# Kernel optimization log

Hardware: AMD Instinct MI355X
Metric: run time of the kernel (lower is better)

Reference implementation:

```python
import jax, jax.numpy as jnp
import numpy as np

N = 100000
E = 3200000

def gcn_conv(x, W, b, src, dst, num_nodes):
    # PyG GCNConv: x' = D^-1/2 (A+I) D^-1/2 (x W) + b
    h = x @ W  # [N, out]
    # self loops appended
    src_sl = jnp.concatenate([src, jnp.arange(num_nodes)])
    dst_sl = jnp.concatenate([dst, jnp.arange(num_nodes)])
    deg = jnp.zeros((num_nodes,), h.dtype).at[dst_sl].add(1.0)
    dinv = jnp.where(deg > 0, 1.0 / jnp.sqrt(deg), 0.0)
    norm = dinv[src_sl] * dinv[dst_sl]  # [E+N]
    msgs = h[src_sl] * norm[:, None]
    out = jnp.zeros_like(h).at[dst_sl].add(msgs)
    return out + b

def setup_inputs() -> dict:
    key = jax.random.key(0)
    k1, k2, k3, k4, k5 = jax.random.split(key, 5)
    z = jax.random.normal(k1, (N, 16), dtype=jnp.float32)
    edge_index = jax.random.randint(k2, (2, E), 0, N, dtype=jnp.int64)
    W1 = jax.random.normal(k3, (16, 256), dtype=jnp.float32) * (1.0 / np.sqrt(16))
    b1 = jnp.zeros((256,), jnp.float32)
    W2 = jax.random.normal(k4, (256, 256), dtype=jnp.float32) * (1.0 / np.sqrt(256))
    b2 = jnp.zeros((256,), jnp.float32)
    return {"z": z, "edge_index": edge_index, "W1": W1, "b1": b1, "W2": W2, "b2": b2}

def reference(z, edge_index, W1, b1, W2, b2):
    src, dst = edge_index[0], edge_index[1]
    h = gcn_conv(z, W1, b1, src, dst, N)
    h = gcn_conv(h, W2, b2, src, dst, N)
    value = jnp.sum(h[src] * h[dst], axis=1)  # [E]
    return jax.nn.sigmoid(value)
```

## Files before the change

kernel.cpp:

```cpp
#include <hip/hip_runtime.h>
#include <hip/hip_fp16.h>
#include <math.h>

#define N_NODES 100000
#define N_EDGES 3200000
#define GRID_N 391
#define GRID_G 6250
#define NSB 782
#define SB_NODES 128
#define SBCAP 5120
#define E_BLK 12800
#define PART_BLOCKS 250
#define PART_THREADS 1024
#define QUART_E 800000
#define GRID_D 3125

#define OFF_DINV 0
#define OFF_C    100016
#define OFF_ZS16 200032
#define OFF_T16  1000048
#define OFF_U    1800064
#define OFF_YT   3400080
#define OFF_ST   4200080
#define OFF_PR   6604720
#define OFF_PB   6604736
#define OFF_ABG  6604752
#define OFF_L    6604768
#define FLOAT_TOTAL 6605024
#define IOFF_GCUR 0
#define IOFF_BEG  1024
#define IOFF_CNT  101024
#define IOFF_BUF  201024
#define IOFF_CSR  4204864

__device__ inline float4 h4_to_f4(uint2 v) {
    __half2 a = *reinterpret_cast<__half2*>(&v.x);
    __half2 b = *reinterpret_cast<__half2*>(&v.y);
    float2 fa = __half22float2(a), fb = __half22float2(b);
    return make_float4(fa.x, fa.y, fb.x, fb.y);
}
__device__ inline uint2 f4_to_h4(float4 f) {
    uint2 r;
    __half2 a = __floats2half2_rn(f.x, f.y);
    __half2 b = __floats2half2_rn(f.z, f.w);
    r.x = *reinterpret_cast<unsigned*>(&a);
    r.y = *reinterpret_cast<unsigned*>(&b);
    return r;
}
__device__ inline float4 pack_h8(float4 a, float4 b) {
    float4 r;
    __half2* p = reinterpret_cast<__half2*>(&r);
    p[0] = __floats2half2_rn(a.x, a.y);
    p[1] = __floats2half2_rn(a.z, a.w);
    p[2] = __floats2half2_rn(b.x, b.y);
    p[3] = __floats2half2_rn(b.z, b.w);
    return r;
}
__device__ inline unsigned h2bits(float a, float b) {
    __half2 h = __floats2half2_rn(a, b);
    return *reinterpret_cast<unsigned*>(&h);
}
__device__ inline float2 bits2f2(unsigned v) {
    __half2 h = *reinterpret_cast<__half2*>(&v);
    return __half22float2(h);
}
__device__ inline float hdot8f(float4 a, float4 b) {
    const __half2* pa = reinterpret_cast<const __half2*>(&a);
    const __half2* pb = reinterpret_cast<const __half2*>(&b);
    float s = 0.0f;
    #pragma unroll
    for (int i = 0; i < 4; i++) {
        float2 fa = __half22float2(pa[i]);
        float2 fb = __half22float2(pb[i]);
        s += fa.x * fb.x + fa.y * fb.y;
    }
    return s;
}

__global__ void __launch_bounds__(PART_THREADS)
k_part(const int* __restrict__ src, const int* __restrict__ dst,
       int* __restrict__ gcur, int* __restrict__ buf) {
    __shared__ int hist[4][NSB];
    __shared__ int cur[NSB];
    int t = threadIdx.x;
    int cp = t >> 8;
    int base = blockIdx.x * E_BLK;
    for (int i = t; i < 4 * NSB; i += PART_THREADS) ((int*)hist)[i] = 0;
    __syncthreads();
    for (int i = t; i < E_BLK; i += PART_THREADS) {
        int e = base + i;
        if (e < N_EDGES)
            atomicAdd(&hist[cp][__builtin_nontemporal_load(dst + e) >> 7], 1);
    }
    __syncthreads();
    for (int i = t; i < NSB; i += PART_THREADS) {
        int h = hist[0][i] + hist[1][i] + hist[2][i] + hist[3][i];
        cur[i] = (h > 0) ? atomicAdd(&gcur[i], h) : 0;
    }
    __syncthreads();
    for (int i = t; i < E_BLK; i += PART_THREADS) {
        int e = base + i;
        if (e >= N_EDGES) continue;
        int d = __builtin_nontemporal_load(dst + e);
        int s = __builtin_nontemporal_load(src + e);
        int sb = d >> 7;
        int pos = atomicAdd(&cur[sb], 1);
        if (pos < SBCAP) buf[sb * SBCAP + pos] = s | ((d & 127) << 17);
    }
}

__global__ void k_sort(const float* __restrict__ z, const int* __restrict__ gcur,
                       const int* __restrict__ buf, int* __restrict__ csr,
                       int* __restrict__ begA, int* __restrict__ cntA,
                       float* __restrict__ ws) {
    __shared__ int pay[SBCAP];
    __shared__ int h[SB_NODES + 1];
    __shared__ int lcur[SB_NODES];
    __shared__ float sdv[SB_NODES];
    int sb = blockIdx.x, t = threadIdx.x;
    int n = gcur[sb];
    if (n > SBCAP) n = SBCAP;
    for (int i = t; i < n; i += 256) pay[i] = buf[sb * SBCAP + i];
    if (t <= SB_NODES) h[t] = 0;
    __syncthreads();
    for (int i = t; i < n; i += 256) atomicAdd(&h[(pay[i] >> 17) + 1], 1);
    __syncthreads();
    int mydeg = 0;
    if (t < SB_NODES) { mydeg = h[t + 1]; h[t + 1] = (mydeg + 3) & ~3; }
    __syncthreads();
    for (int off = 1; off <= SB_NODES; off <<= 1) {
        int v = 0;
        if (t <= SB_NODES && t >= off) v = h[t - off];
        __syncthreads();
        if (t <= SB_NODES) h[t] += v;
        __syncthreads();
    }
    int n0 = sb * SB_NODES;
    if (t < SB_NODES) {
        lcur[t] = h[t];
        float dv = rsqrtf((float)(mydeg + 1));
        sdv[t] = dv;
        if (n0 + t < N_NODES) {
            cntA[n0 + t] = mydeg;
            begA[n0 + t] = sb * SBCAP + h[t];
            ws[OFF_DINV + n0 + t] = dv;
        }
    }
    __syncthreads();
    {
        int nl = t >> 1, half = t & 1;
        int node = n0 + nl;
        if (node < N_NODES) {
            const float4* zr = (const float4*)(z + (size_t)node * 16) + 2 * half;
            float dv = sdv[nl];
            float4 a = zr[0], b = zr[1];
            a = make_float4(a.x * dv, a.y * dv, a.z * dv, a.w * dv);
            b = make_float4(b.x * dv, b.y * dv, b.z * dv, b.w * dv);
            ((float4*)((__half*)(ws + OFF_ZS16) + (size_t)node * 16))[half] = pack_h8(a, b);
        }
    }
    for (int i = t; i < n; i += 256) {
        int p = pay[i];
        int dl = p >> 17;
        int pos = atomicAdd(&lcur[dl], 1);
        if (pos < SBCAP) csr[sb * SBCAP + pos] = p & 0x1FFFF;
    }
}

__global__ void k_gather1(const int* __restrict__ cntA, const int* __restrict__ begA,
                          const int* __restrict__ csr, float* __restrict__ ws) {
    int lane = threadIdx.x & 15;
    int g = threadIdx.x >> 4;
    int q = lane & 3;
    int sub = lane >> 2;
    int d = blockIdx.x * 16 + g;
    if (d >= N_NODES) return;
    const float* dinv = ws + OFF_DINV;
    const __half* zs = (const __half*)(ws + OFF_ZS16);
    float dd = dinv[d];
    float dv2 = dd * dd;
    int deg = cntA[d];
    int beg = begA[d];
    float4 acc = make_float4(0.f, 0.f, 0.f, 0.f);
    float csum = 0.0f;
    int j = 0;
    for (; j + 16 <= deg; j += 16) {
        int4 idx = *(const int4*)(csr + beg + j + sub * 4);
        float4 f0 = h4_to_f4(((const uint2*)(zs + (size_t)idx.x * 16))[q]);
        float4 f1 = h4_to_f4(((const uint2*)(zs + (size_t)idx.y * 16))[q]);
        float4 f2 = h4_to_f4(((const uint2*)(zs + (size_t)idx.z * 16))[q]);
        float4 f3 = h4_to_f4(((const uint2*)(zs + (size_t)idx.w * 16))[q]);
        acc.x += (f0.x + f1.x) + (f2.x + f3.x);
        acc.y += (f0.y + f1.y) + (f2.y + f3.y);
        acc.z += (f0.z + f1.z) + (f2.z + f3.z);
        acc.w += (f0.w + f1.w) + (f2.w + f3.w);
        if (q == 0) csum += (dinv[idx.x] + dinv[idx.y]) + (dinv[idx.z] + dinv[idx.w]);
    }
    for (int t = j + sub; t < deg; t += 4) {
        int s0 = csr[beg + t];
        float4 f0 = h4_to_f4(((const uint2*)(zs + (size_t)s0 * 16))[q]);
        acc.x += f0.x; acc.y += f0.y; acc.z += f0.z; acc.w += f0.w;
        if (q == 0) csum += dinv[s0];
    }
    #pragma unroll
    for (int off = 4; off <= 8; off <<= 1) {
        acc.x += __shfl_xor(acc.x, off, 64);
        acc.y += __shfl_xor(acc.y, off, 64);
        acc.z += __shfl_xor(acc.z, off, 64);
        acc.w += __shfl_xor(acc.w, off, 64);
        csum  += __shfl_xor(csum,  off, 64);
    }
    if (sub == 0) {
        float4 zrow = h4_to_f4(((const uint2*)(zs + (size_t)d * 16))[q]);
        float4 o = make_float4(dv2 * (acc.x + zrow.x), dv2 * (acc.y + zrow.y),
                               dv2 * (acc.z + zrow.z), dv2 * (acc.w + zrow.w));
        ((uint2*)((__half*)(ws + OFF_T16) + (size_t)d * 16))[q] = f4_to_h4(o);
        if (q == 0) (ws + OFF_C)[d] = dd * csum + dv2;
    }
}

__global__ void k_gather2(const int* __restrict__ cntA, const int* __restrict__ begA,
                          const int* __restrict__ csr, float* __restrict__ ws) {
    int lane = threadIdx.x & 15;
    int g = threadIdx.x >> 4;
    int q = lane & 3;
    int sub = lane >> 2;
    int d = blockIdx.x * 16 + g;
    if (d >= N_NODES) return;
    const float* dinv = ws + OFF_DINV;
    const __half* t16 = (const __half*)(ws + OFF_T16);
    float dd = dinv[d];
    int deg = cntA[d];
    int beg = begA[d];
    float4 acc = make_float4(0.f, 0.f, 0.f, 0.f);
    int j = 0;
    for (; j + 16 <= deg; j += 16) {
        int4 idx = *(const int4*)(csr + beg + j + sub * 4);
        float4 f0 = h4_to_f4(((const uint2*)(t16 + (size_t)idx.x * 16))[q]);
        float4 f1 = h4_to_f4(((const uint2*)(t16 + (size_t)idx.y * 16))[q]);
        float4 f2 = h4_to_f4(((const uint2*)(t16 + (size_t)idx.z * 16))[q]);
        float4 f3 = h4_to_f4(((const uint2*)(t16 + (size_t)idx.w * 16))[q]);
        acc.x += (f0.x + f1.x) + (f2.x + f3.x);
        acc.y += (f0.y + f1.y) + (f2.y + f3.y);
        acc.z += (f0.z + f1.z) + (f2.z + f3.z);
        acc.w += (f0.w + f1.w) + (f2.w + f3.w);
    }
    for (int t = j + sub; t < deg; t += 4) {
        int s0 = csr[beg + t];
        float4 f0 = h4_to_f4(((const uint2*)(t16 + (size_t)s0 * 16))[q]);
        acc.x += f0.x; acc.y += f0.y; acc.z += f0.z; acc.w += f0.w;
    }
    #pragma unroll
    for (int off = 4; off <= 8; off <<= 1) {
        acc.x += __shfl_xor(acc.x, off, 64);
        acc.y += __shfl_xor(acc.y, off, 64);
        acc.z += __shfl_xor(acc.z, off, 64);
        acc.w += __shfl_xor(acc.w, off, 64);
    }
    if (sub == 0) {
        float4 trow = h4_to_f4(((const uint2*)(t16 + (size_t)d * 16))[q]);
        float4 o = make_float4(dd * (acc.x + trow.x), dd * (acc.y + trow.y),
                               dd * (acc.z + trow.z), dd * (acc.w + trow.w));
        ((float4*)(ws + OFF_U + (size_t)d * 16))[q] = o;
    }
}

__global__ void k_consts(const float* __restrict__ W1, const float* __restrict__ b1,
                         const float* __restrict__ W2, const float* __restrict__ b2,
                         float* __restrict__ ws, int* __restrict__ gcur) {
    __shared__ float sW1t[16 * 256];
    __shared__ float sM[16 * 257];
    __shared__ float sb1[256], sb2[256], sR[256];
    __shared__ float sG[256], sLf[256];
    int tid = threadIdx.x;
    for (int i = tid; i < 1024; i += 256) gcur[i] = 0;
    #pragma unroll
    for (int r = 0; r < 16; r++)
        sW1t[tid * 16 + r] = W1[r * 256 + tid];
    sb1[tid] = b1[tid];
    sb2[tid] = b2[tid];
    __syncthreads();
    {
        float acc[16];
        #pragma unroll
        for (int i = 0; i < 16; i++) acc[i] = 0.0f;
        float raccv = 0.0f;
        for (int kk = 0; kk < 256; kk += 8) {
            float w2v[8];
            #pragma unroll
            for (int u = 0; u < 8; u++)
                w2v[u] = W2[(kk + u) * 256 + tid];
            #pragma unroll
            for (int u = 0; u < 8; u++) {
                #pragma unroll
                for (int i = 0; i < 16; i++)
                    acc[i] += sW1t[(kk + u) * 16 + i] * w2v[u];
                raccv += sb1[kk + u] * w2v[u];
            }
        }
        #pragma unroll
        for (int i = 0; i < 16; i++) sM[i * 257 + tid] = acc[i];
        sR[tid] = raccv;
    }
    __syncthreads();
    {
        int i = tid >> 4, j = tid & 15;
        float gg = 0.0f;
        for (int t = 0; t < 256; t++) gg += sM[i * 257 + t] * sM[j * 257 + t];
        sG[tid] = gg;
    }
    if (tid < 16) {
        float a = 0.0f, b = 0.0f;
        for (int t = 0; t < 256; t++) {
            a += sM[tid * 257 + t] * sR[t];
            b += sM[tid * 257 + t] * sb2[t];
        }
        ws[OFF_PR + tid] = a;
        ws[OFF_PB + tid] = b;
    }
    if (tid == 0) {
        float al = 0.0f, be = 0.0f, ga = 0.0f;
        for (int t = 0; t < 256; t++) {
            al += sR[t] * sR[t];
            be += sR[t] * sb2[t];
            ga += sb2[t] * sb2[t];
        }
        float disc = sqrtf(al * al + 4.0f);
        float lp = 0.5f * (al + disc);
        float lm = 0.5f * (al - disc);
        float k1 = sqrtf(lp / (lp * lp + 1.0f));
        float k2 = sqrtf(-lm / (lm * lm + 1.0f));
        ws[OFF_ABG + 0] = be;
        ws[OFF_ABG + 1] = 0.5f * ga;
        ws[OFF_ABG + 2] = lp;
        ws[OFF_ABG + 3] = lm;
        ws[OFF_ABG + 4] = k1;
        ws[OFF_ABG + 5] = k2;
    }
    __syncthreads();
    sLf[tid] = 0.0f;
    __syncthreads();
    if (tid == 0) {
        for (int i = 0; i < 16; i++) {
            for (int j = 0; j <= i; j++) {
                float s = sG[i * 16 + j];
                for (int k = 0; k < j; k++) s -= sLf[i * 16 + k] * sLf[j * 16 + k];
                if (i == j) sLf[i * 16 + j] = sqrtf(fmaxf(s, 1e-20f));
                else        sLf[i * 16 + j] = s / sLf[j * 16 + j];
            }
        }
    }
    __syncthreads();
    ws[OFF_L + tid] = sLf[tid];
}

__global__ void k_pack(float* __restrict__ ws) {
    __shared__ float sL[256];
    __shared__ float spr[16];
    __shared__ float spb[16];
    __shared__ float sprm[8];
    int tid = threadIdx.x;
    sL[tid] = ws[OFF_L + tid];
    if (tid < 16) { spr[tid] = ws[OFF_PR + tid]; spb[tid] = ws[OFF_PB + tid]; }
    if (tid < 8) sprm[tid] = ws[OFF_ABG + tid];
    __syncthreads();
    int i = blockIdx.x * blockDim.x + tid;
    if (i >= N_NODES) return;
    const float* u = ws + OFF_U;
    const float* c = ws + OFF_C;
    float ur[16];
    const float4* urow = (const float4*)(u + (size_t)i * 16);
    #pragma unroll
    for (int m = 0; m < 4; m++) {
        float4 a = urow[m];
        ur[4 * m + 0] = a.x; ur[4 * m + 1] = a.y;
        ur[4 * m + 2] = a.z; ur[4 * m + 3] = a.w;
    }
    float A = 0.0f, B = 0.0f;
    #pragma unroll
    for (int kk = 0; kk < 16; kk++) { A += ur[kk] * spr[kk]; B += ur[kk] * spb[kk]; }
    float y[16];
    #pragma unroll
    for (int j = 0; j < 16; j++) {
        float accv = 0.0f;
        #pragma unroll
        for (int kk = 0; kk < 16; kk++) accv += ur[kk] * sL[kk * 16 + j];
        y[j] = accv;
    }
    float beta = sprm[0], gh = sprm[1], lp = sprm[2], lm = sprm[3];
    float k1 = sprm[4], k2 = sprm[5];
    float ci = c[i];
    float Ap = A + beta;
    float Bp = B + gh;
    float r1 = k1 * (lp * ci + Ap);
    float r2 = k2 * (lm * ci + Ap);
    const float inv_s2 = 0.70710678118654752f;
    float r3 = (Bp + 1.0f) * inv_s2;
    float r4 = (Bp - 1.0f) * inv_s2;
    float4* yt = (float4*)(ws + OFF_YT);
    yt[2 * i]     = pack_h8(make_float4(y[0], y[1], y[2], y[3]),
                            make_float4(y[4], y[5], y[6], y[7]));
    yt[2 * i + 1] = pack_h8(make_float4(y[8], y[9], y[10], y[11]),
                            make_float4(y[12], y[13], y[14], y[15]));
    ((uint2*)(ws + OFF_ST))[i] = make_uint2(h2bits(r1, r2), h2bits(r3, r4));
}

__global__ void k_decode(const int* __restrict__ src, const int* __restrict__ dst,
                         const float* __restrict__ ws, float* __restrict__ out) {
    int e0 = blockIdx.x * blockDim.x + threadIdx.x;
    if (e0 >= QUART_E) return;
    const float4* yt = (const float4*)(ws + OFF_YT);
    const uint2*  st = (const uint2*)(ws + OFF_ST);
    int s[4], d[4];
    #pragma unroll
    for (int k = 0; k < 4; k++) {
        int e = e0 + k * QUART_E;
        s[k] = __builtin_nontemporal_load(src + e);
        d[k] = __builtin_nontemporal_load(dst + e);
    }
    float4 sy0[4], sy1[4], dy0[4], dy1[4];
    uint2 ssc[4], dsc[4];
    #pragma unroll
    for (int k = 0; k < 4; k++) {
        sy0[k] = yt[2 * (size_t)s[k]];
        sy1[k] = yt[2 * (size_t)s[k] + 1];
        dy0[k] = yt[2 * (size_t)d[k]];
        dy1[k] = yt[2 * (size_t)d[k] + 1];
        ssc[k] = st[s[k]];
        dsc[k] = st[d[k]];
    }
    #pragma unroll
    for (int k = 0; k < 4; k++) {
        float v = hdot8f(sy0[k], dy0[k]) + hdot8f(sy1[k], dy1[k]);
        float2 ra = bits2f2(ssc[k].x), rb = bits2f2(dsc[k].x);
        float2 rc = bits2f2(ssc[k].y), rd = bits2f2(dsc[k].y);
        v += ra.x * rb.x - ra.y * rb.y + rc.x * rd.x - rc.y * rd.y;
        __builtin_nontemporal_store(1.0f / (1.0f + expf(-v)), out + e0 + k * QUART_E);
    }
}

extern "C" void kernel_launch(void* const* d_in, const int* in_sizes, int n_in,
                              void* d_out, int out_size, void* d_ws, size_t ws_size,
                              hipStream_t stream) {
    const float* z  = (const float*)d_in[0];
    const int*   ei = (const int*)d_in[1];
    const float* W1 = (const float*)d_in[2];
    const float* b1 = (const float*)d_in[3];
    const float* W2 = (const float*)d_in[4];
    const float* b2 = (const float*)d_in[5];
    float* out = (float*)d_out;
    float* ws  = (float*)d_ws;
    int*   wi  = (int*)(ws + FLOAT_TOTAL);

    const int* src = ei;
    const int* dst = ei + N_EDGES;

    int* gcur = wi + IOFF_GCUR;
    int* begA = wi + IOFF_BEG;
    int* cntA = wi + IOFF_CNT;
    int* buf  = wi + IOFF_BUF;
    int* csr  = wi + IOFF_CSR;

    k_consts  <<<1, 256, 0, stream>>>(W1, b1, W2, b2, ws, gcur);
    k_part    <<<PART_BLOCKS, PART_THREADS, 0, stream>>>(src, dst, gcur, buf);
    k_sort    <<<NSB, 256, 0, stream>>>(z, gcur, buf, csr, begA, cntA, ws);
    k_gather1 <<<GRID_G, 256, 0, stream>>>(cntA, begA, csr, ws);
    k_gather2 <<<GRID_G, 256, 0, stream>>>(cntA, begA, csr, ws);
    k_pack    <<<GRID_N, 256, 0, stream>>>(ws);
    k_decode  <<<GRID_D, 256, 0, stream>>>(src, dst, ws, out);
}
```

Measured before the change: 337.2 us.

## Merge constants kernel into partition launch and interleave per-node decode records

The single-block constants computation now runs as an extra block of the partition kernel, sharing its shared memory via a union, and gcur is zeroed with an async memset. This removes a serial prelude launch and lets the constants overlap with edge partitioning. Per-node half-precision features and scale terms are packed into one 64-byte record, so each decode gather touches one contiguous region instead of two arrays. Padding enlarges per-node storage slightly, and the merged block runs with most threads idle.

After: 299.4 us. 1.13x faster.

```diff
diff --git a/kernel.cpp b/kernel.cpp
--- a/kernel.cpp
+++ b/kernel.cpp
@@ -21,7 +21,6 @@
 #define OFF_T16  1000048
 #define OFF_U    1800064
 #define OFF_YT   3400080
-#define OFF_ST   4200080
 #define OFF_PR   6604720
 #define OFF_PB   6604736
 #define OFF_ABG  6604752
@@ -77,25 +76,133 @@
     return s;
 }
 
+struct ConstsSh {
+    float sW1t[16 * 256];
+    float sM[16 * 257];
+    float sb1[256];
+    float sb2[256];
+    float sR[256];
+    float sG[256];
+    float sLf[256];
+};
+struct PartSh {
+    int hist[4][NSB];
+    int cur[NSB];
+};
+
 __global__ void __launch_bounds__(PART_THREADS)
 k_part(const int* __restrict__ src, const int* __restrict__ dst,
-       int* __restrict__ gcur, int* __restrict__ buf) {
-    __shared__ int hist[4][NSB];
-    __shared__ int cur[NSB];
+       int* __restrict__ gcur, int* __restrict__ buf,
+       const float* __restrict__ W1, const float* __restrict__ b1,
+       const float* __restrict__ W2, const float* __restrict__ b2,
+       float* __restrict__ ws) {
+    __shared__ union { ConstsSh c; PartSh p; } sh;
     int t = threadIdx.x;
+
+    if (blockIdx.x == PART_BLOCKS) {
+        bool act = t < 256;
+        if (act) {
+            #pragma unroll
+            for (int r = 0; r < 16; r++)
+                sh.c.sW1t[t * 16 + r] = W1[r * 256 + t];
+            sh.c.sb1[t] = b1[t];
+            sh.c.sb2[t] = b2[t];
+        }
+        __syncthreads();
+        if (act) {
+            float acc[16];
+            #pragma unroll
+            for (int i = 0; i < 16; i++) acc[i] = 0.0f;
+            float raccv = 0.0f;
+            for (int kk = 0; kk < 256; kk += 8) {
+                float w2v[8];
+                #pragma unroll
+                for (int u = 0; u < 8; u++)
+                    w2v[u] = W2[(kk + u) * 256 + t];
+                #pragma unroll
+                for (int u = 0; u < 8; u++) {
+                    #pragma unroll
+                    for (int i = 0; i < 16; i++)
+                        acc[i] += sh.c.sW1t[(kk + u) * 16 + i] * w2v[u];
+                    raccv += sh.c.sb1[kk + u] * w2v[u];
+                }
+            }
+            #pragma unroll
+            for (int i = 0; i < 16; i++) sh.c.sM[i * 257 + t] = acc[i];
+            sh.c.sR[t] = raccv;
+        }
+        __syncthreads();
+        if (act) {
+            int i = t >> 4, j = t & 15;
+            float gg = 0.0f;
+            for (int tt = 0; tt < 256; tt++)
+                gg += sh.c.sM[i * 257 + tt] * sh.c.sM[j * 257 + tt];
+            sh.c.sG[t] = gg;
+        }
+        if (t < 16) {
+            float a = 0.0f, b = 0.0f;
+            for (int tt = 0; tt < 256; tt++) {
+                a += sh.c.sM[t * 257 + tt] * sh.c.sR[tt];
+                b += sh.c.sM[t * 257 + tt] * sh.c.sb2[tt];
+            }
+            ws[OFF_PR + t] = a;
+            ws[OFF_PB + t] = b;
+        }
+        if (t == 0) {
+            float al = 0.0f, be = 0.0f, ga = 0.0f;
+            for (int tt = 0; tt < 256; tt++) {
+                al += sh.c.sR[tt] * sh.c.sR[tt];
+                be += sh.c.sR[tt] * sh.c.sb2[tt];
+                ga += sh.c.sb2[tt] * sh.c.sb2[tt];
+            }
+            float disc = sqrtf(al * al + 4.0f);
+            float lp = 0.5f * (al + disc);
+            float lm = 0.5f * (al - disc);
+            float k1 = sqrtf(lp / (lp * lp + 1.0f));
+            float k2 = sqrtf(-lm / (lm * lm + 1.0f));
+            ws[OFF_ABG + 0] = be;
+            ws[OFF_ABG + 1] = 0.5f * ga;
+            ws[OFF_ABG + 2] = lp;
+            ws[OFF_ABG + 3] = lm;
+            ws[OFF_ABG + 4] = k1;
+            ws[OFF_ABG + 5] = k2;
+        }
+        __syncthreads();
+        if (act) sh.c.sLf[t] = 0.0f;
+        __syncthreads();
+        for (int j = 0; j < 16; j++) {
+            if (t == j) {
+                float s = sh.c.sG[j * 16 + j];
+                for (int k = 0; k < j; k++)
+                    s -= sh.c.sLf[j * 16 + k] * sh.c.sLf[j * 16 + k];
+                sh.c.sLf[j * 16 + j] = sqrtf(fmaxf(s, 1e-20f));
+            }
+            __syncthreads();
+            if (t > j && t < 16) {
+                float s = sh.c.sG[t * 16 + j];
+                for (int k = 0; k < j; k++)
+                    s -= sh.c.sLf[t * 16 + k] * sh.c.sLf[j * 16 + k];
+                sh.c.sLf[t * 16 + j] = s / sh.c.sLf[j * 16 + j];
+            }
+            __syncthreads();
+        }
+        if (act) ws[OFF_L + t] = sh.c.sLf[t];
+        return;
+    }
+
     int cp = t >> 8;
     int base = blockIdx.x * E_BLK;
-    for (int i = t; i < 4 * NSB; i += PART_THREADS) ((int*)hist)[i] = 0;
+    for (int i = t; i < 4 * NSB; i += PART_THREADS) ((int*)sh.p.hist)[i] = 0;
     __syncthreads();
     for (int i = t; i < E_BLK; i += PART_THREADS) {
         int e = base + i;
         if (e < N_EDGES)
-            atomicAdd(&hist[cp][__builtin_nontemporal_load(dst + e) >> 7], 1);
+            atomicAdd(&sh.p.hist[cp][__builtin_nontemporal_load(dst + e) >> 7], 1);
     }
     __syncthreads();
     for (int i = t; i < NSB; i += PART_THREADS) {
-        int h = hist[0][i] + hist[1][i] + hist[2][i] + hist[3][i];
-        cur[i] = (h > 0) ? atomicAdd(&gcur[i], h) : 0;
+        int h = sh.p.hist[0][i] + sh.p.hist[1][i] + sh.p.hist[2][i] + sh.p.hist[3][i];
+        sh.p.cur[i] = (h > 0) ? atomicAdd(&gcur[i], h) : 0;
     }
     __syncthreads();
     for (int i = t; i < E_BLK; i += PART_THREADS) {
@@ -104,7 +211,7 @@
         int d = __builtin_nontemporal_load(dst + e);
         int s = __builtin_nontemporal_load(src + e);
         int sb = d >> 7;
-        int pos = atomicAdd(&cur[sb], 1);
+        int pos = atomicAdd(&sh.p.cur[sb], 1);
         if (pos < SBCAP) buf[sb * SBCAP + pos] = s | ((d & 127) << 17);
     }
 }
@@ -265,95 +372,6 @@
     }
 }
 
-__global__ void k_consts(const float* __restrict__ W1, const float* __restrict__ b1,
-                         const float* __restrict__ W2, const float* __restrict__ b2,
-                         float* __restrict__ ws, int* __restrict__ gcur) {
-    __shared__ float sW1t[16 * 256];
-    __shared__ float sM[16 * 257];
-    __shared__ float sb1[256], sb2[256], sR[256];
-    __shared__ float sG[256], sLf[256];
-    int tid = threadIdx.x;
-    for (int i = tid; i < 1024; i += 256) gcur[i] = 0;
-    #pragma unroll
-    for (int r = 0; r < 16; r++)
-        sW1t[tid * 16 + r] = W1[r * 256 + tid];
-    sb1[tid] = b1[tid];
-    sb2[tid] = b2[tid];
-    __syncthreads();
-    {
-        float acc[16];
-        #pragma unroll
-        for (int i = 0; i < 16; i++) acc[i] = 0.0f;
-        float raccv = 0.0f;
-        for (int kk = 0; kk < 256; kk += 8) {
-            float w2v[8];
-            #pragma unroll
-            for (int u = 0; u < 8; u++)
-                w2v[u] = W2[(kk + u) * 256 + tid];
-            #pragma unroll
-            for (int u = 0; u < 8; u++) {
-                #pragma unroll
-                for (int i = 0; i < 16; i++)
-                    acc[i] += sW1t[(kk + u) * 16 + i] * w2v[u];
-                raccv += sb1[kk + u] * w2v[u];
-            }
-        }
-        #pragma unroll
-        for (int i = 0; i < 16; i++) sM[i * 257 + tid] = acc[i];
-        sR[tid] = raccv;
-    }
-    __syncthreads();
-    {
-        int i = tid >> 4, j = tid & 15;
-        float gg = 0.0f;
-        for (int t = 0; t < 256; t++) gg += sM[i * 257 + t] * sM[j * 257 + t];
-        sG[tid] = gg;
-    }
-    if (tid < 16) {
-        float a = 0.0f, b = 0.0f;
-        for (int t = 0; t < 256; t++) {
-            a += sM[tid * 257 + t] * sR[t];
-            b += sM[tid * 257 + t] * sb2[t];
-        }
-        ws[OFF_PR + tid] = a;
-        ws[OFF_PB + tid] = b;
-    }
-    if (tid == 0) {
-        float al = 0.0f, be = 0.0f, ga = 0.0f;
-        for (int t = 0; t < 256; t++) {
-            al += sR[t] * sR[t];
-            be += sR[t] * sb2[t];
-            ga += sb2[t] * sb2[t];
-        }
-        float disc = sqrtf(al * al + 4.0f);
-        float lp = 0.5f * (al + disc);
-        float lm = 0.5f * (al - disc);
-        float k1 = sqrtf(lp / (lp * lp + 1.0f));
-        float k2 = sqrtf(-lm / (lm * lm + 1.0f));
-        ws[OFF_ABG + 0] = be;
-        ws[OFF_ABG + 1] = 0.5f * ga;
-        ws[OFF_ABG + 2] = lp;
-        ws[OFF_ABG + 3] = lm;
-        ws[OFF_ABG + 4] = k1;
-        ws[OFF_ABG + 5] = k2;
-    }
-    __syncthreads();
-    sLf[tid] = 0.0f;
-    __syncthreads();
-    if (tid == 0) {
-        for (int i = 0; i < 16; i++) {
-            for (int j = 0; j <= i; j++) {
-                float s = sG[i * 16 + j];
-                for (int k = 0; k < j; k++) s -= sLf[i * 16 + k] * sLf[j * 16 + k];
-                if (i == j) sLf[i * 16 + j] = sqrtf(fmaxf(s, 1e-20f));
-                else        sLf[i * 16 + j] = s / sLf[j * 16 + j];
-            }
-        }
-    }
-    __syncthreads();
-    ws[OFF_L + tid] = sLf[tid];
-}
-
 __global__ void k_pack(float* __restrict__ ws) {
     __shared__ float sL[256];
     __shared__ float spr[16];
@@ -397,12 +415,12 @@
     const float inv_s2 = 0.70710678118654752f;
     float r3 = (Bp + 1.0f) * inv_s2;
     float r4 = (Bp - 1.0f) * inv_s2;
-    float4* yt = (float4*)(ws + OFF_YT);
-    yt[2 * i]     = pack_h8(make_float4(y[0], y[1], y[2], y[3]),
-                            make_float4(y[4], y[5], y[6], y[7]));
-    yt[2 * i + 1] = pack_h8(make_float4(y[8], y[9], y[10], y[11]),
-                            make_float4(y[12], y[13], y[14], y[15]));
-    ((uint2*)(ws + OFF_ST))[i] = make_uint2(h2bits(r1, r2), h2bits(r3, r4));
+    float4* rec = (float4*)(ws + OFF_YT) + 4 * (size_t)i;
+    rec[0] = pack_h8(make_float4(y[0], y[1], y[2], y[3]),
+                     make_float4(y[4], y[5], y[6], y[7]));
+    rec[1] = pack_h8(make_float4(y[8], y[9], y[10], y[11]),
+                     make_float4(y[12], y[13], y[14], y[15]));
+    *(uint2*)(rec + 2) = make_uint2(h2bits(r1, r2), h2bits(r3, r4));
 }
 
 __global__ void k_decode(const int* __restrict__ src, const int* __restrict__ dst,
@@ -410,7 +428,6 @@
     int e0 = blockIdx.x * blockDim.x + threadIdx.x;
     if (e0 >= QUART_E) return;
     const float4* yt = (const float4*)(ws + OFF_YT);
-    const uint2*  st = (const uint2*)(ws + OFF_ST);
     int s[4], d[4];
     #pragma unroll
     for (int k = 0; k < 4; k++) {
@@ -422,12 +439,14 @@
     uint2 ssc[4], dsc[4];
     #pragma unroll
     for (int k = 0; k < 4; k++) {
-        sy0[k] = yt[2 * (size_t)s[k]];
-        sy1[k] = yt[2 * (size_t)s[k] + 1];
-        dy0[k] = yt[2 * (size_t)d[k]];
-        dy1[k] = yt[2 * (size_t)d[k] + 1];
-        ssc[k] = st[s[k]];
-        dsc[k] = st[d[k]];
+        const float4* rs = yt + 4 * (size_t)s[k];
+        const float4* rd = yt + 4 * (size_t)d[k];
+        sy0[k] = rs[0];
+        sy1[k] = rs[1];
+        ssc[k] = *(const uint2*)(rs + 2);
+        dy0[k] = rd[0];
+        dy1[k] = rd[1];
+        dsc[k] = *(const uint2*)(rd + 2);
     }
     #pragma unroll
     for (int k = 0; k < 4; k++) {
@@ -461,8 +480,9 @@
     int* buf  = wi + IOFF_BUF;
     int* csr  = wi + IOFF_CSR;
 
-    k_consts  <<<1, 256, 0, stream>>>(W1, b1, W2, b2, ws, gcur);
-    k_part    <<<PART_BLOCKS, PART_THREADS, 0, stream>>>(src, dst, gcur, buf);
+    hipMemsetAsync(gcur, 0, 1024 * sizeof(int), stream);
+    k_part    <<<PART_BLOCKS + 1, PART_THREADS, 0, stream>>>(src, dst, gcur, buf,
+                                                             W1, b1, W2, b2, ws);
     k_sort    <<<NSB, 256, 0, stream>>>(z, gcur, buf, csr, begA, cntA, ws);
     k_gather1 <<<GRID_G, 256, 0, stream>>>(cntA, begA, csr, ws);
     k_gather2 <<<GRID_G, 256, 0, stream>>>(cntA, begA, csr, ws);
```
